# Kernel optimization log

Measured on AMD Instinct MI355X. Metric: run time of the kernel, lower is better.

The kernel has to match this reference:

```python
import jax, jax.numpy as jnp
import numpy as np

M, N, K = 1024, 11008, 4096


def _unpack_i2u(Bp):
    """Unpack 2-bit unsigned weights per decode_i2u_to_i8s interleave.

    Bp: [N, K//4] int8 storage. Within each group of 4 bytes (16 elements),
    output element at position 4*i + j = (byte_j >> (2*i)) & 3.
    Returns [N, K] int8 with values in {0,1,2,3}.
    """
    Bu = jax.lax.bitcast_convert_type(Bp, jnp.uint8)  # [N, K//4]
    n, kc = Bu.shape
    Bg = Bu.reshape(n, kc // 4, 1, 4)                 # [N, G, 1, j]
    shifts = (jnp.arange(4, dtype=jnp.uint8) * jnp.uint8(2)).reshape(1, 1, 4, 1)
    vals = (Bg >> shifts) & jnp.uint8(3)              # [N, G, i, j]
    return vals.reshape(n, kc * 4).astype(jnp.int8)   # [N, K]


def setup_inputs() -> dict:
    key = jax.random.key(0)
    k1, k2 = jax.random.split(key)
    A = jax.random.randint(k1, (M, K), -128, 128, dtype=jnp.int8)
    B = jax.random.randint(k2, (N, K // 4), -128, 128, dtype=jnp.int8)
    return {"A": A, "B": B}


def reference(A, B):
    W = _unpack_i2u(B)  # [N, K] int8
    C = jax.lax.dot_general(
        A, W,
        dimension_numbers=(((1,), (1,)), ((), ())),
        preferred_element_type=jnp.int32,
    )  # [M, N] int32
    return C
```

## Files before the change

### kernel.cpp

```cpp
#include <hip/hip_runtime.h>
#include <stdint.h>


#define MM 1024
#define NN 11008
#define KK 4096
#define KSTEPS 64
#define MTILES (MM / 128)
#define NTILES (NN / 128)

using i32x4  = __attribute__((ext_vector_type(4))) int;
using i32x16 = __attribute__((ext_vector_type(16))) int;

__device__ __forceinline__ int pack4(i32x4 v) {
    return (int)(((uint32_t)v[0] & 0xFFu) | (((uint32_t)v[1] & 0xFFu) << 8)
               | (((uint32_t)v[2] & 0xFFu) << 16) | (((uint32_t)v[3] & 0xFFu) << 24));
}

__global__ __launch_bounds__(256) void prep_A(const int* __restrict__ src,
                                              uint8_t* __restrict__ dst) {
    const int g = blockIdx.x * 256 + threadIdx.x;
    const int kstep = g >> 12;
    const int rem   = g & 4095;
    const int mtile = rem >> 9;
    const int c     = rem & 511;
    const int row32 = (c >> 7) & 3, kk2 = (c >> 6) & 1;
    const int lane  = c & 63;
    const int row   = mtile * 128 + row32 * 32 + (lane & 31);
    const int kbyte = kstep * 64 + kk2 * 32 + (lane >> 5) * 16;
    const i32x4* s4 = (const i32x4*)(src + (size_t)row * KK + kbyte);
    i32x4 o;
#pragma unroll
    for (int q = 0; q < 4; ++q) o[q] = pack4(s4[q]);
    *(i32x4*)(dst + (size_t)g * 16) = o;
}

__global__ __launch_bounds__(256) void prep_B(const int* __restrict__ src,
                                              uint8_t* __restrict__ dst) {
    const int t = blockIdx.x * 256 + threadIdx.x;
    const int lane = t & 63;
    const int wc   = (t >> 6) & 1;
    const int rem  = t >> 7;
    const int ntile = rem % NTILES;
    const int kstep = rem / NTILES;
    const int l31 = lane & 31, h = lane >> 5;
    i32x4 o;
#pragma unroll
    for (int q = 0; q < 4; ++q) {
        const int ni = q >> 1, kk2 = q & 1;
        const int n  = ntile * 128 + wc * 64 + ni * 32 + l31;
        const i32x4 v = *(const i32x4*)(src + (size_t)n * (KK / 4) + kstep * 16 + kk2 * 8 + h * 4);
        o[q] = pack4(v);
    }
    *(i32x4*)(dst + (size_t)t * 16) = o;
}

__global__ __launch_bounds__(256, 3) void bitnet_gemm(const uint8_t* __restrict__ A2,
                                                      const uint8_t* __restrict__ B3,
                                                      int* __restrict__ C) {
    const int t    = threadIdx.x;
    const int lane = t & 63, wave = t >> 6;
    const int wr   = wave >> 1, wc = wave & 1;
    const int l31  = lane & 31, h = lane >> 5;
    const int by   = blockIdx.y, bx = blockIdx.x;

    const size_t strideA = (size_t)MTILES * 8192;
    const size_t strideB = (size_t)NTILES * 2048;

    const uint8_t* pa[4];
#pragma unroll
    for (int s = 0; s < 4; ++s) {
        const int mi = s >> 1, kk2 = s & 1;
        pa[s] = A2 + (size_t)by * 8192 + ((wr * 2 + mi) * 2 + kk2) * 1024 + lane * 16;
    }
    const uint8_t* pb = B3 + (size_t)bx * 2048 + wc * 1024 + lane * 16;

    i32x16 acc[2][2] = {};
    i32x4 fa0[4], fa1[4], fa2[4], fa3[4];
    i32x4 fp0, fp1, fp2, fp3;

    auto LOAD = [&](i32x4 (&a)[4], i32x4& p, int ks) {
#pragma unroll
        for (int s = 0; s < 4; ++s)
            a[s] = *(const i32x4*)(pa[s] + (size_t)ks * strideA);
        p = *(const i32x4*)(pb + (size_t)ks * strideB);
    };

    auto COMPUTE = [&](const i32x4 (&a)[4], const i32x4& p) {
#pragma unroll
        for (int kk2 = 0; kk2 < 2; ++kk2) {
            const uint32_t q0 = (uint32_t)p[kk2];
            const uint32_t q1 = (uint32_t)p[2 + kk2];
            i32x4 b0, b1;
#pragma unroll
            for (int i = 0; i < 4; ++i) {
                b0[i] = (int)((q0 >> (2 * i)) & 0x03030303u);
                b1[i] = (int)((q1 >> (2 * i)) & 0x03030303u);
            }
            acc[0][0] = __builtin_amdgcn_mfma_i32_32x32x32_i8(a[0 * 2 + kk2], b0, acc[0][0], 0, 0, 0);
            acc[0][1] = __builtin_amdgcn_mfma_i32_32x32x32_i8(a[0 * 2 + kk2], b1, acc[0][1], 0, 0, 0);
            acc[1][0] = __builtin_amdgcn_mfma_i32_32x32x32_i8(a[1 * 2 + kk2], b0, acc[1][0], 0, 0, 0);
            acc[1][1] = __builtin_amdgcn_mfma_i32_32x32x32_i8(a[1 * 2 + kk2], b1, acc[1][1], 0, 0, 0);
        }
    };

    LOAD(fa0, fp0, 0);
    LOAD(fa1, fp1, 1);
    LOAD(fa2, fp2, 2);
    LOAD(fa3, fp3, 3);

#pragma unroll 1
    for (int ks = 0; ks < KSTEPS - 4; ks += 4) {
        COMPUTE(fa0, fp0); LOAD(fa0, fp0, ks + 4);
        COMPUTE(fa1, fp1); LOAD(fa1, fp1, ks + 5);
        COMPUTE(fa2, fp2); LOAD(fa2, fp2, ks + 6);
        COMPUTE(fa3, fp3); LOAD(fa3, fp3, ks + 7);
    }
    COMPUTE(fa0, fp0);
    COMPUTE(fa1, fp1);
    COMPUTE(fa2, fp2);
    COMPUTE(fa3, fp3);

    const int brow = by * 128, bcol = bx * 128;
#pragma unroll
    for (int mi = 0; mi < 2; ++mi)
#pragma unroll
        for (int ni = 0; ni < 2; ++ni) {
            const int colg = bcol + wc * 64 + ni * 32 + l31;
#pragma unroll
            for (int r = 0; r < 16; ++r) {
                const int rowin = (r & 3) + 8 * (r >> 2) + 4 * h;
                const int rowg  = brow + wr * 64 + mi * 32 + rowin;
                C[(size_t)rowg * NN + colg] = acc[mi][ni][r];
            }
        }
}

extern "C" void kernel_launch(void* const* d_in, const int* in_sizes, int n_in,
                              void* d_out, int out_size, void* d_ws, size_t ws_size,
                              hipStream_t stream) {
    const int* A32 = (const int*)d_in[0];
    const int* B32 = (const int*)d_in[1];
    int* C = (int*)d_out;

    uint8_t* A2 = (uint8_t*)d_ws;
    uint8_t* B3 = A2 + (size_t)MM * KK;

    prep_A<<<dim3((MM * KK / 16) / 256), dim3(256), 0, stream>>>(A32, A2);
    prep_B<<<dim3((NN * 64) / 256), dim3(256), 0, stream>>>(B32, B3);
    bitnet_gemm<<<dim3(NTILES, MTILES), dim3(256), 0, stream>>>(A2, B3, C);
}
```

Before: 73.14 us.

## Switch GEMM to single-wave blocks with 64x128 wave tiles and XCD-aware mapping

Each workgroup becomes one wave that computes a 64x128 output tile (2x4 MFMA accumulators), up from 64x64 per wave inside 4-wave blocks. Block IDs are remapped so consecutive IDs (likely spread round-robin over the chiplets) cover neighbouring tiles that share data. Prefetch depth drops from 4 to 2 k-steps to fit the larger accumulator set. The aim is more reuse of each B fragment and fewer loads per MFMA. The cost is higher register pressure, less latency hiding and possibly lower occupancy.

```diff
diff --git a/kernel.cpp b/kernel.cpp
--- a/kernel.cpp
+++ b/kernel.cpp
@@ -8,6 +8,7 @@
 #define KSTEPS 64
 #define MTILES (MM / 128)
 #define NTILES (NN / 128)
+#define NWAVES (16 * NTILES)
 
 using i32x4  = __attribute__((ext_vector_type(4))) int;
 using i32x16 = __attribute__((ext_vector_type(16))) int;
@@ -55,14 +56,19 @@
     *(i32x4*)(dst + (size_t)t * 16) = o;
 }
 
-__global__ __launch_bounds__(256, 3) void bitnet_gemm(const uint8_t* __restrict__ A2,
-                                                      const uint8_t* __restrict__ B3,
-                                                      int* __restrict__ C) {
-    const int t    = threadIdx.x;
-    const int lane = t & 63, wave = t >> 6;
-    const int wr   = wave >> 1, wc = wave & 1;
+struct Bfrag { i32x4 c0, c1; };
+
+__global__ __launch_bounds__(64, 2) void bitnet_gemm(const uint8_t* __restrict__ A2,
+                                                     const uint8_t* __restrict__ B3,
+                                                     int* __restrict__ C) {
+    const int lane = threadIdx.x;
     const int l31  = lane & 31, h = lane >> 5;
-    const int by   = blockIdx.y, bx = blockIdx.x;
+
+    const int bid = blockIdx.x;
+    const int l   = (bid & 7) * (NWAVES / 8) + (bid >> 3);
+    const int wm  = l & 15;
+    const int wn  = l >> 4;
+    const int mtile = wm >> 1, half = wm & 1;
 
     const size_t strideA = (size_t)MTILES * 8192;
     const size_t strideB = (size_t)NTILES * 2048;
@@ -71,67 +77,60 @@
 #pragma unroll
     for (int s = 0; s < 4; ++s) {
         const int mi = s >> 1, kk2 = s & 1;
-        pa[s] = A2 + (size_t)by * 8192 + ((wr * 2 + mi) * 2 + kk2) * 1024 + lane * 16;
+        pa[s] = A2 + (size_t)mtile * 8192 + ((half * 2 + mi) * 2 + kk2) * 1024 + lane * 16;
     }
-    const uint8_t* pb = B3 + (size_t)bx * 2048 + wc * 1024 + lane * 16;
+    const uint8_t* pb = B3 + (size_t)wn * 2048 + lane * 16;
 
-    i32x16 acc[2][2] = {};
-    i32x4 fa0[4], fa1[4], fa2[4], fa3[4];
-    i32x4 fp0, fp1, fp2, fp3;
+    i32x16 acc[2][4] = {};
+    i32x4 fa0[4], fa1[4];
+    Bfrag fp0, fp1;
 
-    auto LOAD = [&](i32x4 (&a)[4], i32x4& p, int ks) {
+    auto LOAD = [&](i32x4 (&a)[4], Bfrag& p, int ks) {
 #pragma unroll
         for (int s = 0; s < 4; ++s)
             a[s] = *(const i32x4*)(pa[s] + (size_t)ks * strideA);
-        p = *(const i32x4*)(pb + (size_t)ks * strideB);
+        p.c0 = *(const i32x4*)(pb + (size_t)ks * strideB);
+        p.c1 = *(const i32x4*)(pb + (size_t)ks * strideB + 1024);
     };
 
-    auto COMPUTE = [&](const i32x4 (&a)[4], const i32x4& p) {
+    auto COMPUTE = [&](const i32x4 (&a)[4], const Bfrag& p) {
 #pragma unroll
         for (int kk2 = 0; kk2 < 2; ++kk2) {
-            const uint32_t q0 = (uint32_t)p[kk2];
-            const uint32_t q1 = (uint32_t)p[2 + kk2];
-            i32x4 b0, b1;
 #pragma unroll
-            for (int i = 0; i < 4; ++i) {
-                b0[i] = (int)((q0 >> (2 * i)) & 0x03030303u);
-                b1[i] = (int)((q1 >> (2 * i)) & 0x03030303u);
+            for (int nc = 0; nc < 4; ++nc) {
+                const uint32_t q = (uint32_t)((nc < 2 ? p.c0 : p.c1)[(nc & 1) * 2 + kk2]);
+                i32x4 b;
+#pragma unroll
+                for (int i = 0; i < 4; ++i)
+                    b[i] = (int)((q >> (2 * i)) & 0x03030303u);
+                acc[0][nc] = __builtin_amdgcn_mfma_i32_32x32x32_i8(a[0 + kk2], b, acc[0][nc], 0, 0, 0);
+                acc[1][nc] = __builtin_amdgcn_mfma_i32_32x32x32_i8(a[2 + kk2], b, acc[1][nc], 0, 0, 0);
             }
-            acc[0][0] = __builtin_amdgcn_mfma_i32_32x32x32_i8(a[0 * 2 + kk2], b0, acc[0][0], 0, 0, 0);
-            acc[0][1] = __builtin_amdgcn_mfma_i32_32x32x32_i8(a[0 * 2 + kk2], b1, acc[0][1], 0, 0, 0);
-            acc[1][0] = __builtin_amdgcn_mfma_i32_32x32x32_i8(a[1 * 2 + kk2], b0, acc[1][0], 0, 0, 0);
-            acc[1][1] = __builtin_amdgcn_mfma_i32_32x32x32_i8(a[1 * 2 + kk2], b1, acc[1][1], 0, 0, 0);
         }
     };
 
     LOAD(fa0, fp0, 0);
     LOAD(fa1, fp1, 1);
-    LOAD(fa2, fp2, 2);
-    LOAD(fa3, fp3, 3);
 
 #pragma unroll 1
-    for (int ks = 0; ks < KSTEPS - 4; ks += 4) {
-        COMPUTE(fa0, fp0); LOAD(fa0, fp0, ks + 4);
-        COMPUTE(fa1, fp1); LOAD(fa1, fp1, ks + 5);
-        COMPUTE(fa2, fp2); LOAD(fa2, fp2, ks + 6);
-        COMPUTE(fa3, fp3); LOAD(fa3, fp3, ks + 7);
+    for (int ks = 0; ks < KSTEPS - 2; ks += 2) {
+        COMPUTE(fa0, fp0); LOAD(fa0, fp0, ks + 2);
+        COMPUTE(fa1, fp1); LOAD(fa1, fp1, ks + 3);
     }
     COMPUTE(fa0, fp0);
     COMPUTE(fa1, fp1);
-    COMPUTE(fa2, fp2);
-    COMPUTE(fa3, fp3);
 
-    const int brow = by * 128, bcol = bx * 128;
+    const int brow = wm * 64, bcol = wn * 128;
 #pragma unroll
     for (int mi = 0; mi < 2; ++mi)
 #pragma unroll
-        for (int ni = 0; ni < 2; ++ni) {
-            const int colg = bcol + wc * 64 + ni * 32 + l31;
+        for (int nc = 0; nc < 4; ++nc) {
+            const int colg = bcol + nc * 32 + l31;
 #pragma unroll
             for (int r = 0; r < 16; ++r) {
                 const int rowin = (r & 3) + 8 * (r >> 2) + 4 * h;
-                const int rowg  = brow + wr * 64 + mi * 32 + rowin;
-                C[(size_t)rowg * NN + colg] = acc[mi][ni][r];
+                const int rowg  = brow + mi * 32 + rowin;
+                C[(size_t)rowg * NN + colg] = acc[mi][nc][r];
             }
         }
 }
@@ -148,5 +147,5 @@
 
     prep_A<<<dim3((MM * KK / 16) / 256), dim3(256), 0, stream>>>(A32, A2);
     prep_B<<<dim3((NN * 64) / 256), dim3(256), 0, stream>>>(B32, B3);
-    bitnet_gemm<<<dim3(NTILES, MTILES), dim3(256), 0, stream>>>(A2, B3, C);
+    bitnet_gemm<<<dim3(NWAVES), dim3(64), 0, stream>>>(A2, B3, C);
 }
```

Result: faster. 69.84 us (-4.5%).
